# Optimization experiments

Measured on AMD Instinct MI355X. Metric: run time of the kernel, lower is better.

Reference implementation:

```python
import jax, jax.numpy as jnp
import numpy as np

N_NODES = 50000
N_EDGES = 800000
IN_DIM = 256
OUT_DIM = 64
NEG_SLOPE = 0.01  # torch F.leaky_relu default


def setup_inputs() -> dict:
    key = jax.random.key(0)
    k1, k2, k3, k4, k5 = jax.random.split(key, 5)
    h = jax.random.normal(k1, (N_NODES, IN_DIM), dtype=jnp.float32)
    W = jax.random.normal(k2, (OUT_DIM, IN_DIM), dtype=jnp.float32) * 0.05
    a = jax.random.normal(k3, (1, 2 * OUT_DIM), dtype=jnp.float32) * 0.05
    src = jax.random.randint(k4, (N_EDGES,), 0, N_NODES)
    dst = jax.random.randint(k5, (N_EDGES,), 0, N_NODES)
    return {"h": h, "W": W, "a": a, "src": src, "dst": dst}


def reference(h, W, a, src, dst):
    # node projection: z = fc(h)               [N, D_out]
    z = jnp.einsum("ni,oi->no", h, W)
    # edge attention: e = leaky_relu(attn_fc(concat(z_src, z_dst)))
    # split a into left/right halves to avoid materializing the [E, 2D] concat
    a_l, a_r = a[0, :OUT_DIM], a[0, OUT_DIM:]
    el = z @ a_l  # [N]
    er = z @ a_r  # [N]
    e = jax.nn.leaky_relu(el[src] + er[dst], negative_slope=NEG_SLOPE)  # [E]
    # segment softmax over incoming edges of each destination node
    m = jax.ops.segment_max(e, dst, num_segments=N_NODES)  # [N], -inf for isolated
    ex = jnp.exp(e - m[dst])                               # [E]
    s = jax.ops.segment_sum(ex, dst, num_segments=N_NODES)  # [N]
    alpha = ex / s[dst]                                     # [E]
    # weighted-sum aggregation of source features
    h_out = jax.ops.segment_sum(alpha[:, None] * z[src], dst, num_segments=N_NODES)
    return h_out
```

## Files before the change

### kernel.cpp

```cpp
#include <hip/hip_runtime.h>

#define IN_DIM 256
#define OUT_DIM 64
#define NEG_SLOPE 0.01f
#define CHUNK 1024
#define KPT (CHUNK / 256)

typedef __attribute__((ext_vector_type(8))) short short8v;
typedef __attribute__((ext_vector_type(4))) float float4v;

__device__ __forceinline__ unsigned short f2bf(float f) {
    unsigned u = __float_as_uint(f);
    return (unsigned short)((u + 0x7FFFu + ((u >> 16) & 1u)) >> 16);
}
__device__ __forceinline__ float bf2f(unsigned short u) {
    return __uint_as_float((unsigned)u << 16);
}

__global__ void k_init(const float* __restrict__ W, unsigned short* __restrict__ Wb,
                       int* __restrict__ bc, int* __restrict__ cursor) {
    int i = blockIdx.x * blockDim.x + threadIdx.x;
    if (i < OUT_DIM * IN_DIM) Wb[i] = f2bf(W[i]);
    if (i < 256) { bc[i] = 0; cursor[i] = 0; }
}

__global__ __launch_bounds__(256, 3) void k1_mfma_count(
        const float* __restrict__ h, const unsigned short* __restrict__ Wb,
        const float* __restrict__ a, const int* __restrict__ dst,
        unsigned short* __restrict__ zb, float* __restrict__ el, float* __restrict__ er,
        int* __restrict__ bc, int M, int E) {
    __shared__ uint4 wlds[2048];
    __shared__ int hist[256];
    hist[threadIdx.x] = 0;

    #pragma unroll
    for (int k = 0; k < 8; ++k) {
        int c = threadIdx.x + k * 256;
        int row = c >> 5, col = c & 31;
        wlds[(row << 5) | (col ^ (row & 7))] = ((const uint4*)Wb)[c];
    }
    __syncthreads();

    const int lane = threadIdx.x & 63;
    const int wid  = (blockIdx.x * 256 + threadIdx.x) >> 6;
    const int r0 = wid * 16;

    if (r0 < M) {
        const int lrow = lane & 15;
        const int kgrp = lane >> 4;
        const int k0   = kgrp * 8;
        const int swz  = lrow & 7;

        const float* __restrict__ hrow = h + (size_t)(r0 + lrow) * IN_DIM;

        float4 hreg[16];
        #pragma unroll
        for (int s = 0; s < 8; ++s) {
            hreg[2 * s]     = *(const float4*)(hrow + s * 32 + k0);
            hreg[2 * s + 1] = *(const float4*)(hrow + s * 32 + k0 + 4);
        }

        float4v acc[4];
        #pragma unroll
        for (int n = 0; n < 4; ++n) acc[n] = (float4v){0.f, 0.f, 0.f, 0.f};

        #pragma unroll
        for (int s = 0; s < 8; ++s) {
            float4 ha = hreg[2 * s], hb = hreg[2 * s + 1];
            short8v afrag;
            afrag[0] = (short)f2bf(ha.x); afrag[1] = (short)f2bf(ha.y);
            afrag[2] = (short)f2bf(ha.z); afrag[3] = (short)f2bf(ha.w);
            afrag[4] = (short)f2bf(hb.x); afrag[5] = (short)f2bf(hb.y);
            afrag[6] = (short)f2bf(hb.z); afrag[7] = (short)f2bf(hb.w);
            #pragma unroll
            for (int n = 0; n < 4; ++n) {
                const int slot = ((n * 16 + lrow) << 5) | ((s * 4 + kgrp) ^ swz);
                short8v bfrag = *(const short8v*)&wlds[slot];
                acc[n] = __builtin_amdgcn_mfma_f32_16x16x32_bf16(afrag, bfrag, acc[n], 0, 0, 0);
            }
        }

        float al4[4], ar4[4];
        #pragma unroll
        for (int n = 0; n < 4; ++n) {
            al4[n] = a[n * 16 + lrow];
            ar4[n] = a[OUT_DIM + n * 16 + lrow];
        }
        #pragma unroll
        for (int j = 0; j < 4; ++j) {
            const int row = r0 + kgrp * 4 + j;
            float vl = 0.f, vr = 0.f;
            #pragma unroll
            for (int n = 0; n < 4; ++n) {
                float v = acc[n][j];
                zb[(size_t)row * OUT_DIM + n * 16 + lrow] = f2bf(v);
                vl += v * al4[n];
                vr += v * ar4[n];
            }
            #pragma unroll
            for (int m = 8; m >= 1; m >>= 1) {
                vl += __shfl_xor(vl, m, 64);
                vr += __shfl_xor(vr, m, 64);
            }
            if (lrow == 0) { el[row] = vl; er[row] = vr; }
        }
    }

    __syncthreads();
    const int stride = gridDim.x * 256;
    for (int i = blockIdx.x * 256 + threadIdx.x; i < E; i += stride)
        atomicAdd(&hist[dst[i] >> 8], 1);
    __syncthreads();
    if (hist[threadIdx.x]) atomicAdd(&bc[threadIdx.x], hist[threadIdx.x]);
}

__global__ __launch_bounds__(256) void kA_scatter(
        const int* __restrict__ src, const int* __restrict__ dst,
        const int* __restrict__ bc, int* __restrict__ cursor,
        unsigned* __restrict__ bucketbuf, int E, int nbuck) {
    __shared__ unsigned stag[CHUNK];
    __shared__ int bsc[256], cnt[256], lofs[256], lcur[256], tb[256];
    const int t = threadIdx.x;
    const int base = blockIdx.x * CHUNK;
    const int n = min(CHUNK, E - base);

    int bv = (t < nbuck) ? bc[t] : 0;
    bsc[t] = bv;
    cnt[t] = 0;
    __syncthreads();
    for (int off = 1; off < 256; off <<= 1) {
        int add = (t >= off) ? bsc[t - off] : 0;
        __syncthreads();
        bsc[t] += add;
        __syncthreads();
    }
    const int bstart_t = bsc[t] - bv;

    int es[KPT], ed[KPT];
    #pragma unroll
    for (int k = 0; k < KPT; ++k) {
        int p = t + k * 256;
        if (p < n) {
            es[k] = src[base + p];
            ed[k] = dst[base + p];
            atomicAdd(&cnt[ed[k] >> 8], 1);
        }
    }
    __syncthreads();

    lofs[t] = cnt[t];
    __syncthreads();
    for (int off = 1; off < 256; off <<= 1) {
        int add = (t >= off) ? lofs[t - off] : 0;
        __syncthreads();
        lofs[t] += add;
        __syncthreads();
    }
    lofs[t] -= cnt[t];
    __syncthreads();

    {
        int c = cnt[t];
        int g = c ? atomicAdd(&cursor[t], c) : 0;
        tb[t] = bstart_t + g - lofs[t];
    }
    lcur[t] = lofs[t];
    __syncthreads();

    #pragma unroll
    for (int k = 0; k < KPT; ++k) {
        int p = t + k * 256;
        if (p < n) {
            int b = ed[k] >> 8;
            int pos = atomicAdd(&lcur[b], 1);
            stag[pos] = ((unsigned)ed[k] << 16) | (unsigned)es[k];
        }
    }
    __syncthreads();

    #pragma unroll
    for (int k = 0; k < KPT; ++k) {
        int p = t + k * 256;
        if (p < n) {
            unsigned v = stag[p];
            int b = v >> 24;
            bucketbuf[tb[b] + p] = v;
        }
    }
}

__global__ __launch_bounds__(256) void kB_build(
        const unsigned* __restrict__ bucketbuf, const int* __restrict__ bc,
        int* __restrict__ csr_src, int* __restrict__ ends, int N, int nbuck) {
    __shared__ int sc[256], lcnt[256], lofs[256], lcur[256];
    __shared__ int s_start;
    const int b = blockIdx.x, t = threadIdx.x;

    int bv = (t < nbuck) ? bc[t] : 0;
    sc[t] = bv;
    lcnt[t] = 0;
    __syncthreads();
    for (int off = 1; off < 256; off <<= 1) {
        int add = (t >= off) ? sc[t - off] : 0;
        __syncthreads();
        sc[t] += add;
        __syncthreads();
    }
    if (t == b) s_start = sc[t] - bv;
    __syncthreads();

    const int start = s_start;
    const int cnt = bc[b];
    const int node0 = b << 8;
    const int nloc = min(256, N - node0);

    for (int i = t; i < cnt; i += 256)
        atomicAdd(&lcnt[(bucketbuf[start + i] >> 16) & 255], 1);
    __syncthreads();

    lofs[t] = lcnt[t];
    __syncthreads();
    for (int off = 1; off < 256; off <<= 1) {
        int add = (t >= off) ? lofs[t - off] : 0;
        __syncthreads();
        lofs[t] += add;
        __syncthreads();
    }
    if (t < nloc) ends[node0 + t] = start + lofs[t];
    lcur[t] = lofs[t] - lcnt[t];
    __syncthreads();

    for (int i = t; i < cnt; i += 256) {
        unsigned v = bucketbuf[start + i];
        int node = (v >> 16) & 255;
        int pos = atomicAdd(&lcur[node], 1);
        csr_src[start + pos] = (int)(v & 0xFFFFu);
    }
}

__global__ __launch_bounds__(256) void k5_node(
        const int* __restrict__ csr_src, const int* __restrict__ ends,
        const float* __restrict__ el, const float* __restrict__ er,
        const unsigned short* __restrict__ zb, float* __restrict__ out, int N) {
    const int lane = threadIdx.x & 63;
    const int node = blockIdx.x * 4 + (threadIdx.x >> 6);
    if (node >= N) return;

    const int start = (node == 0) ? 0 : ends[node - 1];
    const int end   = ends[node];
    const int deg   = end - start;
    const int half  = lane >> 5;
    const int lh    = lane & 31;

    float rlo = 0.f, rhi = 0.f;

    if (deg > 0 && deg <= 64) {
        const float er_i = er[node];
        int   s0 = 0;
        float m  = -3.4e38f;
        float e0 = 0.0f;
        if (lane < deg) {
            s0 = csr_src[start + lane];
            float x = el[s0] + er_i;
            e0 = fmaxf(x, NEG_SLOPE * x);
            m  = e0;
        }
        #pragma unroll
        for (int msk = 32; msk; msk >>= 1) m = fmaxf(m, __shfl_xor(m, msk, 64));
        float ex0 = (lane < deg) ? __expf(e0 - m) : 0.0f;
        float sum = ex0;
        #pragma unroll
        for (int msk = 32; msk; msk >>= 1) sum += __shfl_xor(sum, msk, 64);
        const float inv = 1.0f / sum;

        const int npairs = (deg + 1) >> 1;
        float2 acc0 = {0.f, 0.f}, acc1 = {0.f, 0.f},
               acc2 = {0.f, 0.f}, acc3 = {0.f, 0.f};
        int p = 0;
        for (; p + 4 <= npairs; p += 4) {
            #pragma unroll
            for (int q = 0; q < 4; ++q) {
                int e  = 2 * (p + q) + half;
                int cl = (e < deg) ? e : (deg - 1);
                float wv = __shfl(ex0, cl, 64);
                int   sv = __shfl(s0,  cl, 64);
                if (e >= deg) wv = 0.0f;
                unsigned u = *(const unsigned*)(zb + (size_t)sv * OUT_DIM + lh * 2);
                float zl = bf2f((unsigned short)(u & 0xFFFFu));
                float zh = bf2f((unsigned short)(u >> 16));
                if (q == 0) { acc0.x += wv * zl; acc0.y += wv * zh; }
                else if (q == 1) { acc1.x += wv * zl; acc1.y += wv * zh; }
                else if (q == 2) { acc2.x += wv * zl; acc2.y += wv * zh; }
                else { acc3.x += wv * zl; acc3.y += wv * zh; }
            }
        }
        for (; p < npairs; ++p) {
            int e  = 2 * p + half;
            int cl = (e < deg) ? e : (deg - 1);
            float wv = __shfl(ex0, cl, 64);
            int   sv = __shfl(s0,  cl, 64);
            if (e >= deg) wv = 0.0f;
            unsigned u = *(const unsigned*)(zb + (size_t)sv * OUT_DIM + lh * 2);
            acc0.x += wv * bf2f((unsigned short)(u & 0xFFFFu));
            acc0.y += wv * bf2f((unsigned short)(u >> 16));
        }
        rlo = ((acc0.x + acc1.x) + (acc2.x + acc3.x));
        rhi = ((acc0.y + acc1.y) + (acc2.y + acc3.y));
        rlo += __shfl_xor(rlo, 32, 64);
        rhi += __shfl_xor(rhi, 32, 64);
        rlo *= inv; rhi *= inv;
    } else if (deg > 64) {
        const float er_i = er[node];
        float e0 = 0.0f, e1 = 0.0f;
        int   s0 = 0,    s1 = 0;
        float m = -3.4e38f;
        int t = 0;
        for (int j = start + lane; j < end; j += 64, ++t) {
            int s = csr_src[j];
            float x = el[s] + er_i;
            float e = fmaxf(x, NEG_SLOPE * x);
            if (t == 0) { e0 = e; s0 = s; }
            else if (t == 1) { e1 = e; s1 = s; }
            m = fmaxf(m, e);
        }
        #pragma unroll
        for (int msk = 32; msk; msk >>= 1) m = fmaxf(m, __shfl_xor(m, msk, 64));
        float sum = 0.0f;
        t = 0;
        for (int j = start + lane; j < end; j += 64, ++t) {
            float e;
            if (t == 0) e = e0;
            else if (t == 1) e = e1;
            else {
                int s = csr_src[j];
                float x = el[s] + er_i;
                e = fmaxf(x, NEG_SLOPE * x);
            }
            float ex = __expf(e - m);
            if (t == 0) e0 = ex; else if (t == 1) e1 = ex;
            sum += ex;
        }
        #pragma unroll
        for (int msk = 32; msk; msk >>= 1) sum += __shfl_xor(sum, msk, 64);
        const float inv = 1.0f / sum;

        float acc = 0.0f;
        for (int r = 0; r < deg; ++r) {
            int tt = r >> 6, owner = r & 63;
            int s; float ex;
            if (tt == 0)      { s = __shfl(s0, owner, 64); ex = __shfl(e0, owner, 64); }
            else if (tt == 1) { s = __shfl(s1, owner, 64); ex = __shfl(e1, owner, 64); }
            else {
                s = csr_src[start + r];
                float x = el[s] + er_i;
                float e = fmaxf(x, NEG_SLOPE * x);
                ex = __expf(e - m);
            }
            acc += ex * bf2f(zb[(size_t)s * OUT_DIM + lane]);
        }
        acc *= inv;
        rlo = __shfl(acc, 2 * lh, 64);
        rhi = __shfl(acc, 2 * lh + 1, 64);
    }

    if (lane < 32) {
        float2 o; o.x = rlo; o.y = rhi;
        *(float2*)(out + (size_t)node * OUT_DIM + lh * 2) = o;
    }
}

extern "C" void kernel_launch(void* const* d_in, const int* in_sizes, int n_in,
                              void* d_out, int out_size, void* d_ws, size_t ws_size,
                              hipStream_t stream) {
    const float* h   = (const float*)d_in[0];
    const float* W   = (const float*)d_in[1];
    const float* a   = (const float*)d_in[2];
    const int*   src = (const int*)d_in[3];
    const int*   dst = (const int*)d_in[4];
    float* out = (float*)d_out;

    const int N = in_sizes[0] / IN_DIM;
    const int E = in_sizes[3];
    const int nbuck = (N + 255) >> 8;

    unsigned short* zb = (unsigned short*)d_ws;
    float* el   = (float*)(zb + (size_t)N * OUT_DIM);
    float* er   = el + N;
    int*   ends = (int*)(er + N);
    int*   csr_src = ends + N;
    unsigned* bucketbuf = (unsigned*)(csr_src + E);
    int*   bc     = (int*)(bucketbuf + E);
    int*   cursor = bc + 256;
    unsigned short* Wb = (unsigned short*)(cursor + 256);

    k_init<<<(OUT_DIM * IN_DIM + 255) / 256, 256, 0, stream>>>(W, Wb, bc, cursor);
    {
        const int waves = (N + 15) / 16;
        k1_mfma_count<<<(waves + 3) / 4, 256, 0, stream>>>(h, Wb, a, dst, zb, el, er,
                                                           bc, N, E);
    }
    kA_scatter<<<(E + CHUNK - 1) / CHUNK, 256, 0, stream>>>(src, dst, bc, cursor,
                                                            bucketbuf, E, nbuck);
    kB_build<<<nbuck, 256, 0, stream>>>(bucketbuf, bc, csr_src, ends, N, nbuck);
    k5_node<<<(N + 3) / 4, 256, 0, stream>>>(csr_src, ends, el, er, zb, out, N);
}
```

Measured before the change: 97.13 us.

## Merge CSR build stages into one cooperative kernel with grid syncs

```diff
diff --git a/kernel.cpp b/kernel.cpp
--- a/kernel.cpp
+++ b/kernel.cpp
@@ -1,4 +1,7 @@
 #include <hip/hip_runtime.h>
+#include <hip/hip_cooperative_groups.h>
+
+namespace cg = cooperative_groups;
 
 #define IN_DIM 256
 #define OUT_DIM 64
@@ -9,232 +12,221 @@
 typedef __attribute__((ext_vector_type(8))) short short8v;
 typedef __attribute__((ext_vector_type(4))) float float4v;
 
-__device__ __forceinline__ unsigned short f2bf(float f) {
+__device__ __forceinline__ unsigned f2bf(float f) {
     unsigned u = __float_as_uint(f);
-    return (unsigned short)((u + 0x7FFFu + ((u >> 16) & 1u)) >> 16);
+    return (u + 0x7FFFu + ((u >> 16) & 1u)) >> 16;
 }
 __device__ __forceinline__ float bf2f(unsigned short u) {
     return __uint_as_float((unsigned)u << 16);
 }
 
-__global__ void k_init(const float* __restrict__ W, unsigned short* __restrict__ Wb,
-                       int* __restrict__ bc, int* __restrict__ cursor) {
-    int i = blockIdx.x * blockDim.x + threadIdx.x;
-    if (i < OUT_DIM * IN_DIM) Wb[i] = f2bf(W[i]);
-    if (i < 256) { bc[i] = 0; cursor[i] = 0; }
-}
-
-__global__ __launch_bounds__(256, 3) void k1_mfma_count(
-        const float* __restrict__ h, const unsigned short* __restrict__ Wb,
-        const float* __restrict__ a, const int* __restrict__ dst,
+__global__ __launch_bounds__(256, 3) void k1_mfma(
+        const float* __restrict__ h, const float* __restrict__ W,
+        const float* __restrict__ a,
         unsigned short* __restrict__ zb, float* __restrict__ el, float* __restrict__ er,
-        int* __restrict__ bc, int M, int E) {
+        int M) {
     __shared__ uint4 wlds[2048];
-    __shared__ int hist[256];
-    hist[threadIdx.x] = 0;
 
     #pragma unroll
     for (int k = 0; k < 8; ++k) {
         int c = threadIdx.x + k * 256;
         int row = c >> 5, col = c & 31;
-        wlds[(row << 5) | (col ^ (row & 7))] = ((const uint4*)Wb)[c];
+        const float* wsrc = W + c * 8;
+        float4 wa = *(const float4*)wsrc;
+        float4 wb = *(const float4*)(wsrc + 4);
+        uint4 pk;
+        pk.x = f2bf(wa.x) | (f2bf(wa.y) << 16);
+        pk.y = f2bf(wa.z) | (f2bf(wa.w) << 16);
+        pk.z = f2bf(wb.x) | (f2bf(wb.y) << 16);
+        pk.w = f2bf(wb.z) | (f2bf(wb.w) << 16);
+        wlds[(row << 5) | (col ^ (row & 7))] = pk;
     }
     __syncthreads();
 
     const int lane = threadIdx.x & 63;
     const int wid  = (blockIdx.x * 256 + threadIdx.x) >> 6;
     const int r0 = wid * 16;
-
-    if (r0 < M) {
-        const int lrow = lane & 15;
-        const int kgrp = lane >> 4;
-        const int k0   = kgrp * 8;
-        const int swz  = lrow & 7;
-
-        const float* __restrict__ hrow = h + (size_t)(r0 + lrow) * IN_DIM;
-
-        float4 hreg[16];
-        #pragma unroll
-        for (int s = 0; s < 8; ++s) {
-            hreg[2 * s]     = *(const float4*)(hrow + s * 32 + k0);
-            hreg[2 * s + 1] = *(const float4*)(hrow + s * 32 + k0 + 4);
-        }
-
-        float4v acc[4];
-        #pragma unroll
-        for (int n = 0; n < 4; ++n) acc[n] = (float4v){0.f, 0.f, 0.f, 0.f};
-
-        #pragma unroll
-        for (int s = 0; s < 8; ++s) {
-            float4 ha = hreg[2 * s], hb = hreg[2 * s + 1];
-            short8v afrag;
-            afrag[0] = (short)f2bf(ha.x); afrag[1] = (short)f2bf(ha.y);
-            afrag[2] = (short)f2bf(ha.z); afrag[3] = (short)f2bf(ha.w);
-            afrag[4] = (short)f2bf(hb.x); afrag[5] = (short)f2bf(hb.y);
-            afrag[6] = (short)f2bf(hb.z); afrag[7] = (short)f2bf(hb.w);
-            #pragma unroll
-            for (int n = 0; n < 4; ++n) {
-                const int slot = ((n * 16 + lrow) << 5) | ((s * 4 + kgrp) ^ swz);
-                short8v bfrag = *(const short8v*)&wlds[slot];
-                acc[n] = __builtin_amdgcn_mfma_f32_16x16x32_bf16(afrag, bfrag, acc[n], 0, 0, 0);
-            }
-        }
-
-        float al4[4], ar4[4];
+    if (r0 >= M) return;
+
+    const int lrow = lane & 15;
+    const int kgrp = lane >> 4;
+    const int k0   = kgrp * 8;
+    const int swz  = lrow & 7;
+
+    const float* __restrict__ hrow = h + (size_t)(r0 + lrow) * IN_DIM;
+
+    float4 hreg[16];
+    #pragma unroll
+    for (int s = 0; s < 8; ++s) {
+        hreg[2 * s]     = *(const float4*)(hrow + s * 32 + k0);
+        hreg[2 * s + 1] = *(const float4*)(hrow + s * 32 + k0 + 4);
+    }
+
+    float4v acc[4];
+    #pragma unroll
+    for (int n = 0; n < 4; ++n) acc[n] = (float4v){0.f, 0.f, 0.f, 0.f};
+
+    #pragma unroll
+    for (int s = 0; s < 8; ++s) {
+        float4 ha = hreg[2 * s], hb = hreg[2 * s + 1];
+        short8v afrag;
+        afrag[0] = (short)f2bf(ha.x); afrag[1] = (short)f2bf(ha.y);
+        afrag[2] = (short)f2bf(ha.z); afrag[3] = (short)f2bf(ha.w);
+        afrag[4] = (short)f2bf(hb.x); afrag[5] = (short)f2bf(hb.y);
+        afrag[6] = (short)f2bf(hb.z); afrag[7] = (short)f2bf(hb.w);
         #pragma unroll
         for (int n = 0; n < 4; ++n) {
-            al4[n] = a[n * 16 + lrow];
-            ar4[n] = a[OUT_DIM + n * 16 + lrow];
-        }
-        #pragma unroll
-        for (int j = 0; j < 4; ++j) {
-            const int row = r0 + kgrp * 4 + j;
-            float vl = 0.f, vr = 0.f;
-            #pragma unroll
-            for (int n = 0; n < 4; ++n) {
-                float v = acc[n][j];
-                zb[(size_t)row * OUT_DIM + n * 16 + lrow] = f2bf(v);
-                vl += v * al4[n];
-                vr += v * ar4[n];
-            }
-            #pragma unroll
-            for (int m = 8; m >= 1; m >>= 1) {
-                vl += __shfl_xor(vl, m, 64);
-                vr += __shfl_xor(vr, m, 64);
-            }
-            if (lrow == 0) { el[row] = vl; er[row] = vr; }
-        }
-    }
-
+            const int slot = ((n * 16 + lrow) << 5) | ((s * 4 + kgrp) ^ swz);
+            short8v bfrag = *(const short8v*)&wlds[slot];
+            acc[n] = __builtin_amdgcn_mfma_f32_16x16x32_bf16(afrag, bfrag, acc[n], 0, 0, 0);
+        }
+    }
+
+    float al4[4], ar4[4];
+    #pragma unroll
+    for (int n = 0; n < 4; ++n) {
+        al4[n] = a[n * 16 + lrow];
+        ar4[n] = a[OUT_DIM + n * 16 + lrow];
+    }
+    #pragma unroll
+    for (int j = 0; j < 4; ++j) {
+        const int row = r0 + kgrp * 4 + j;
+        float vl = 0.f, vr = 0.f;
+        #pragma unroll
+        for (int n = 0; n < 4; ++n) {
+            float v = acc[n][j];
+            zb[(size_t)row * OUT_DIM + n * 16 + lrow] = (unsigned short)f2bf(v);
+            vl += v * al4[n];
+            vr += v * ar4[n];
+        }
+        #pragma unroll
+        for (int m = 8; m >= 1; m >>= 1) {
+            vl += __shfl_xor(vl, m, 64);
+            vr += __shfl_xor(vr, m, 64);
+        }
+        if (lrow == 0) { el[row] = vl; er[row] = vr; }
+    }
+}
+
+__global__ __launch_bounds__(256) void k_csr(
+        const int* __restrict__ src, const int* __restrict__ dst,
+        int* __restrict__ bc, int* __restrict__ cursor,
+        unsigned* __restrict__ bucketbuf,
+        int* __restrict__ csr_src, int* __restrict__ ends,
+        int N, int E, int nbuck, int nchunk) {
+    __shared__ int bpre[256];
+    __shared__ int t0[256], t1[256], t2[256], t3[256];
+    __shared__ unsigned stag[CHUNK];
+    cg::grid_group grid = cg::this_grid();
+    const int t = threadIdx.x;
+    const int grids = gridDim.x;
+
+    t0[t] = 0;
     __syncthreads();
-    const int stride = gridDim.x * 256;
-    for (int i = blockIdx.x * 256 + threadIdx.x; i < E; i += stride)
-        atomicAdd(&hist[dst[i] >> 8], 1);
+    for (int i = blockIdx.x * 256 + t; i < E; i += grids * 256)
+        atomicAdd(&t0[dst[i] >> 8], 1);
     __syncthreads();
-    if (hist[threadIdx.x]) atomicAdd(&bc[threadIdx.x], hist[threadIdx.x]);
-}
-
-__global__ __launch_bounds__(256) void kA_scatter(
-        const int* __restrict__ src, const int* __restrict__ dst,
-        const int* __restrict__ bc, int* __restrict__ cursor,
-        unsigned* __restrict__ bucketbuf, int E, int nbuck) {
-    __shared__ unsigned stag[CHUNK];
-    __shared__ int bsc[256], cnt[256], lofs[256], lcur[256], tb[256];
-    const int t = threadIdx.x;
-    const int base = blockIdx.x * CHUNK;
-    const int n = min(CHUNK, E - base);
-
-    int bv = (t < nbuck) ? bc[t] : 0;
-    bsc[t] = bv;
-    cnt[t] = 0;
+    if (t0[t]) atomicAdd(&bc[t], t0[t]);
+    grid.sync();
+
+    int bv = bc[t];
+    t0[t] = bv;
     __syncthreads();
     for (int off = 1; off < 256; off <<= 1) {
-        int add = (t >= off) ? bsc[t - off] : 0;
-        __syncthreads();
-        bsc[t] += add;
-        __syncthreads();
-    }
-    const int bstart_t = bsc[t] - bv;
-
-    int es[KPT], ed[KPT];
-    #pragma unroll
-    for (int k = 0; k < KPT; ++k) {
-        int p = t + k * 256;
-        if (p < n) {
-            es[k] = src[base + p];
-            ed[k] = dst[base + p];
-            atomicAdd(&cnt[ed[k] >> 8], 1);
-        }
-    }
+        int add = (t >= off) ? t0[t - off] : 0;
+        __syncthreads();
+        t0[t] += add;
+        __syncthreads();
+    }
+    bpre[t] = t0[t] - bv;
     __syncthreads();
-
-    lofs[t] = cnt[t];
-    __syncthreads();
-    for (int off = 1; off < 256; off <<= 1) {
-        int add = (t >= off) ? lofs[t - off] : 0;
-        __syncthreads();
-        lofs[t] += add;
-        __syncthreads();
-    }
-    lofs[t] -= cnt[t];
-    __syncthreads();
-
-    {
-        int c = cnt[t];
-        int g = c ? atomicAdd(&cursor[t], c) : 0;
-        tb[t] = bstart_t + g - lofs[t];
-    }
-    lcur[t] = lofs[t];
-    __syncthreads();
-
-    #pragma unroll
-    for (int k = 0; k < KPT; ++k) {
-        int p = t + k * 256;
-        if (p < n) {
-            int b = ed[k] >> 8;
-            int pos = atomicAdd(&lcur[b], 1);
-            stag[pos] = ((unsigned)ed[k] << 16) | (unsigned)es[k];
-        }
-    }
-    __syncthreads();
-
-    #pragma unroll
-    for (int k = 0; k < KPT; ++k) {
-        int p = t + k * 256;
-        if (p < n) {
-            unsigned v = stag[p];
-            int b = v >> 24;
-            bucketbuf[tb[b] + p] = v;
-        }
-    }
-}
-
-__global__ __launch_bounds__(256) void kB_build(
-        const unsigned* __restrict__ bucketbuf, const int* __restrict__ bc,
-        int* __restrict__ csr_src, int* __restrict__ ends, int N, int nbuck) {
-    __shared__ int sc[256], lcnt[256], lofs[256], lcur[256];
-    __shared__ int s_start;
-    const int b = blockIdx.x, t = threadIdx.x;
-
-    int bv = (t < nbuck) ? bc[t] : 0;
-    sc[t] = bv;
-    lcnt[t] = 0;
-    __syncthreads();
-    for (int off = 1; off < 256; off <<= 1) {
-        int add = (t >= off) ? sc[t - off] : 0;
-        __syncthreads();
-        sc[t] += add;
-        __syncthreads();
-    }
-    if (t == b) s_start = sc[t] - bv;
-    __syncthreads();
-
-    const int start = s_start;
-    const int cnt = bc[b];
-    const int node0 = b << 8;
-    const int nloc = min(256, N - node0);
-
-    for (int i = t; i < cnt; i += 256)
-        atomicAdd(&lcnt[(bucketbuf[start + i] >> 16) & 255], 1);
-    __syncthreads();
-
-    lofs[t] = lcnt[t];
-    __syncthreads();
-    for (int off = 1; off < 256; off <<= 1) {
-        int add = (t >= off) ? lofs[t - off] : 0;
-        __syncthreads();
-        lofs[t] += add;
-        __syncthreads();
-    }
-    if (t < nloc) ends[node0 + t] = start + lofs[t];
-    lcur[t] = lofs[t] - lcnt[t];
-    __syncthreads();
-
-    for (int i = t; i < cnt; i += 256) {
-        unsigned v = bucketbuf[start + i];
-        int node = (v >> 16) & 255;
-        int pos = atomicAdd(&lcur[node], 1);
-        csr_src[start + pos] = (int)(v & 0xFFFFu);
+    const int bstart_t = bpre[t];
+
+    for (int chunk = blockIdx.x; chunk < nchunk; chunk += grids) {
+        const int base = chunk * CHUNK;
+        const int n = min(CHUNK, E - base);
+
+        t0[t] = 0;
+        __syncthreads();
+        int es[KPT], ed[KPT];
+        #pragma unroll
+        for (int k = 0; k < KPT; ++k) {
+            int p = t + k * 256;
+            if (p < n) {
+                es[k] = src[base + p];
+                ed[k] = dst[base + p];
+                atomicAdd(&t0[ed[k] >> 8], 1);
+            }
+        }
+        __syncthreads();
+        t1[t] = t0[t];
+        __syncthreads();
+        for (int off = 1; off < 256; off <<= 1) {
+            int add = (t >= off) ? t1[t - off] : 0;
+            __syncthreads();
+            t1[t] += add;
+            __syncthreads();
+        }
+        t1[t] -= t0[t];
+        __syncthreads();
+        {
+            int c = t0[t];
+            int g = c ? atomicAdd(&cursor[t], c) : 0;
+            t3[t] = bstart_t + g - t1[t];
+        }
+        t2[t] = t1[t];
+        __syncthreads();
+        #pragma unroll
+        for (int k = 0; k < KPT; ++k) {
+            int p = t + k * 256;
+            if (p < n) {
+                int b = ed[k] >> 8;
+                int pos = atomicAdd(&t2[b], 1);
+                stag[pos] = ((unsigned)ed[k] << 16) | (unsigned)es[k];
+            }
+        }
+        __syncthreads();
+        #pragma unroll
+        for (int k = 0; k < KPT; ++k) {
+            int p = t + k * 256;
+            if (p < n) {
+                unsigned v = stag[p];
+                bucketbuf[t3[v >> 24] + p] = v;
+            }
+        }
+        __syncthreads();
+    }
+    grid.sync();
+
+    for (int b = blockIdx.x; b < nbuck; b += grids) {
+        const int start = bpre[b];
+        const int cnt = bc[b];
+        const int node0 = b << 8;
+        const int nloc = min(256, N - node0);
+
+        t0[t] = 0;
+        __syncthreads();
+        for (int i = t; i < cnt; i += 256)
+            atomicAdd(&t0[(bucketbuf[start + i] >> 16) & 255], 1);
+        __syncthreads();
+        t1[t] = t0[t];
+        __syncthreads();
+        for (int off = 1; off < 256; off <<= 1) {
+            int add = (t >= off) ? t1[t - off] : 0;
+            __syncthreads();
+            t1[t] += add;
+            __syncthreads();
+        }
+        if (t < nloc) ends[node0 + t] = start + t1[t];
+        t2[t] = t1[t] - t0[t];
+        __syncthreads();
+        for (int i = t; i < cnt; i += 256) {
+            unsigned v = bucketbuf[start + i];
+            int node = (v >> 16) & 255;
+            int pos = atomicAdd(&t2[node], 1);
+            csr_src[start + pos] = (int)(v & 0xFFFFu);
+        }
+        __syncthreads();
     }
 }
 
@@ -382,6 +374,7 @@
     const int N = in_sizes[0] / IN_DIM;
     const int E = in_sizes[3];
     const int nbuck = (N + 255) >> 8;
+    const int nchunk = (E + CHUNK - 1) / CHUNK;
 
     unsigned short* zb = (unsigned short*)d_ws;
     float* el   = (float*)(zb + (size_t)N * OUT_DIM);
@@ -391,16 +384,28 @@
     unsigned* bucketbuf = (unsigned*)(csr_src + E);
     int*   bc     = (int*)(bucketbuf + E);
     int*   cursor = bc + 256;
-    unsigned short* Wb = (unsigned short*)(cursor + 256);
-
-    k_init<<<(OUT_DIM * IN_DIM + 255) / 256, 256, 0, stream>>>(W, Wb, bc, cursor);
+
+    hipMemsetAsync(bc, 0, 512 * sizeof(int), stream);
+
     {
         const int waves = (N + 15) / 16;
-        k1_mfma_count<<<(waves + 3) / 4, 256, 0, stream>>>(h, Wb, a, dst, zb, el, er,
-                                                           bc, N, E);
-    }
-    kA_scatter<<<(E + CHUNK - 1) / CHUNK, 256, 0, stream>>>(src, dst, bc, cursor,
-                                                            bucketbuf, E, nbuck);
-    kB_build<<<nbuck, 256, 0, stream>>>(bucketbuf, bc, csr_src, ends, N, nbuck);
+        k1_mfma<<<(waves + 3) / 4, 256, 0, stream>>>(h, W, a, zb, el, er, N);
+    }
+
+    {
+        int occ = 0;
+        if (hipOccupancyMaxActiveBlocksPerMultiprocessor(
+                &occ, (const void*)k_csr, 256, 0) != hipSuccess || occ < 1)
+            occ = 1;
+        int grid = occ * 256;
+        if (grid > nchunk) grid = nchunk;
+        int N_ = N, E_ = E, nb_ = nbuck, nc_ = nchunk;
+        void* args[] = { (void*)&src, (void*)&dst, (void*)&bc, (void*)&cursor,
+                         (void*)&bucketbuf, (void*)&csr_src, (void*)&ends,
+                         (void*)&N_, (void*)&E_, (void*)&nb_, (void*)&nc_ };
+        hipLaunchCooperativeKernel((const void*)k_csr, dim3(grid), dim3(256),
+                                   args, 0, stream);
+    }
+
     k5_node<<<(N + 3) / 4, 256, 0, stream>>>(csr_src, ends, el, er, zb, out, N);
 }
```

After: 234.1 us. +141.0%, slower.
